# Kernel optimization log

Hardware: AMD Instinct MI355X
Metric: run time of the kernel (lower is better)

The kernel has to match this reference:

```python
import jax, jax.numpy as jnp
import numpy as np

N_NODES = 65536
N_EDGES = 1048576
IN_FEATS = 128
H1 = 128
H2 = 256
N_CLASSES = 16


def setup_inputs() -> dict:
    key = jax.random.key(0)
    ks = jax.random.split(key, 12)
    s = 0.05
    x = jax.random.normal(ks[0], (N_NODES, IN_FEATS), dtype=jnp.float32)
    src = jax.random.randint(ks[1], (N_EDGES,), 0, N_NODES, dtype=jnp.int32)
    dst = jax.random.randint(ks[2], (N_EDGES,), 0, N_NODES, dtype=jnp.int32)
    # SAGEConv('pool') params: fc_pool (bias), fc_self (no bias), fc_neigh (no bias), output bias
    Wp = jax.random.normal(ks[3], (H1, IN_FEATS), dtype=jnp.float32) * s
    bp = jnp.zeros((H1,), dtype=jnp.float32)
    Ws = jax.random.normal(ks[4], (H1, IN_FEATS), dtype=jnp.float32) * s
    Wn = jax.random.normal(ks[5], (H1, H1), dtype=jnp.float32) * s
    bn = jnp.zeros((H1,), dtype=jnp.float32)
    # MLP head
    W1 = jax.random.normal(ks[6], (H2, H1), dtype=jnp.float32) * s
    b1 = jnp.zeros((H2,), dtype=jnp.float32)
    W2 = jax.random.normal(ks[7], (N_CLASSES, H2), dtype=jnp.float32) * s
    b2 = jnp.zeros((N_CLASSES,), dtype=jnp.float32)
    return {"x": x, "Wp": Wp, "bp": bp, "Ws": Ws, "Wn": Wn, "bn": bn,
            "W1": W1, "b1": b1, "W2": W2, "b2": b2, "src": src, "dst": dst}


def reference(x, Wp, bp, Ws, Wn, bn, W1, b1, W2, b2, src, dst):
    N = x.shape[0]
    # SAGEConv 'pool': per-edge MLP on gathered source features, segment-max over dst
    m = jax.nn.relu(x[src] @ Wp.T + bp)              # [E, H1]
    pooled = jax.ops.segment_max(m, dst, num_segments=N)  # [N, H1], -inf for isolated
    pooled = jnp.where(jnp.isneginf(pooled), 0.0, pooled)
    h = x @ Ws.T + pooled @ Wn.T + bn                # combine self + neigh
    h = jax.nn.leaky_relu(h)                         # slope 0.01 matches torch default
    h = jax.nn.leaky_relu(h @ W1.T + b1)
    # dropout is identity in eval mode
    h = jax.nn.sigmoid(h @ W2.T + b2)
    return h
```

## Files before the change

kernel.cpp:

```cpp
#include <hip/hip_runtime.h>
#include <cstdint>
#include <cstddef>

typedef __attribute__((ext_vector_type(8))) __bf16 bf16x8;
typedef __attribute__((ext_vector_type(4))) float f32x4;

union bf8pack { unsigned short u[8]; bf16x8 v; uint4 q; };

#define BCAP 768

static __device__ __forceinline__ unsigned short f2b(float f) {
    union { float f; unsigned int u; } v; v.f = f;
    unsigned int u = v.u;
    unsigned int r = (u + 0x7fffu + ((u >> 16) & 1u)) >> 16;
    return (unsigned short)r;
}

static __device__ __forceinline__ bf16x8 cvt8(const float* __restrict__ p) {
    float4 f0 = *(const float4*)p;
    float4 f1 = *(const float4*)(p + 4);
    bf8pack pk;
    pk.u[0] = f2b(f0.x); pk.u[1] = f2b(f0.y);
    pk.u[2] = f2b(f0.z); pk.u[3] = f2b(f0.w);
    pk.u[4] = f2b(f1.x); pk.u[5] = f2b(f1.y);
    pk.u[6] = f2b(f1.z); pk.u[7] = f2b(f1.w);
    return pk.v;
}

static __device__ __forceinline__ unsigned int pkmax(unsigned int a, unsigned int b) {
    unsigned int d;
    asm("v_pk_max_u16 %0, %1, %2" : "=v"(d) : "v"(a), "v"(b));
    return d;
}

__global__ __launch_bounds__(256) void mega0(
    const int* __restrict__ src, const int* __restrict__ dst,
    int* __restrict__ bcnt, unsigned int* __restrict__ pairs,
    const float* __restrict__ x, const float* __restrict__ Wp,
    const float* __restrict__ bp,
    const float* __restrict__ Ws, const float* __restrict__ Wn,
    const float* __restrict__ W1, const float* __restrict__ W2,
    unsigned short* __restrict__ Wcat, unsigned short* __restrict__ W1_b,
    unsigned short* __restrict__ W2_b, unsigned short* __restrict__ y,
    unsigned short* __restrict__ xb)
{
    const int tid = threadIdx.x;
    const int bx = (int)blockIdx.x;

    if (bx < 512) {
        const int bm = bx;
        const int w  = tid >> 6;
        const int wm = w & 1, wn = w >> 1;
        const int l  = tid & 63;
        const int lr = l & 15, quad = l >> 4;
        const int m0 = bm * 128 + wm * 64;
        const int n0 = wn * 64;

        f32x4 acc[4][4];
#pragma unroll
        for (int i = 0; i < 4; i++)
#pragma unroll
            for (int j = 0; j < 4; j++) acc[i][j] = (f32x4){0.f, 0.f, 0.f, 0.f};

        const float* Apf = x  + (size_t)(m0 + lr) * 128 + quad * 8;
        const float* Bpf = Wp + (size_t)(n0 + lr) * 128 + quad * 8;

#pragma unroll
        for (int ks = 0; ks < 4; ks++) {
            bf16x8 af[4], bf[4];
#pragma unroll
            for (int i = 0; i < 4; i++) {
                const float* p = Apf + (size_t)i * 16 * 128 + ks * 32;
                float4 f0 = *(const float4*)p;
                float4 f1 = *(const float4*)(p + 4);
                bf8pack pk;
                pk.u[0] = f2b(f0.x); pk.u[1] = f2b(f0.y);
                pk.u[2] = f2b(f0.z); pk.u[3] = f2b(f0.w);
                pk.u[4] = f2b(f1.x); pk.u[5] = f2b(f1.y);
                pk.u[6] = f2b(f1.z); pk.u[7] = f2b(f1.w);
                af[i] = pk.v;
                if (wn == 0)
                    *(uint4*)(xb + (size_t)(m0 + lr + i * 16) * 128 + ks * 32 + quad * 8) = pk.q;
            }
#pragma unroll
            for (int i = 0; i < 4; i++)
                bf[i] = cvt8(Bpf + (size_t)i * 16 * 128 + ks * 32);
#pragma unroll
            for (int mi = 0; mi < 4; mi++)
#pragma unroll
                for (int ni = 0; ni < 4; ni++)
                    acc[mi][ni] = __builtin_amdgcn_mfma_f32_16x16x32_bf16(
                        af[mi], bf[ni], acc[mi][ni], 0, 0, 0);
        }

#pragma unroll
        for (int ni = 0; ni < 4; ni++) {
            const int col = n0 + ni * 16 + lr;
            const float bv = bp[col];
#pragma unroll
            for (int mi = 0; mi < 4; mi++) {
#pragma unroll
                for (int r = 0; r < 4; r++) {
                    const int row = m0 + mi * 16 + quad * 4 + r;
                    float v = acc[mi][ni][r] + bv;
                    v = v > 0.f ? v : 0.f;
                    y[(size_t)row * 128 + col] = f2b(v);
                }
            }
        }
        return;
    }

    if (bx < 784) {
        int i = (bx - 512) * 256 + tid;
        if (i < 32768) {
            int o = i >> 8, k = i & 255;
            Wcat[i] = f2b(k < 128 ? Ws[o * 128 + k] : Wn[o * 128 + (k - 128)]);
        } else if (i < 65536) {
            W1_b[i - 32768] = f2b(W1[i - 32768]);
        } else {
            W2_b[i - 65536] = f2b(W2[i - 65536]);
        }
        return;
    }

    __shared__ int h[2048];
    __shared__ int base_l[2048];
    __shared__ int cnt[2048];
    for (int i = tid; i < 2048; i += 256) { h[i] = 0; cnt[i] = 0; }
    __syncthreads();
    const int base = (bx - 784) * 4096;
    int d_r[16], s_r[16];
    const int4* s4 = (const int4*)(src + base);
    const int4* d4 = (const int4*)(dst + base);
#pragma unroll
    for (int i = 0; i < 4; i++) {
        int4 dv = d4[tid + i * 256];
        int4 sv = s4[tid + i * 256];
        d_r[i * 4 + 0] = dv.x; d_r[i * 4 + 1] = dv.y;
        d_r[i * 4 + 2] = dv.z; d_r[i * 4 + 3] = dv.w;
        s_r[i * 4 + 0] = sv.x; s_r[i * 4 + 1] = sv.y;
        s_r[i * 4 + 2] = sv.z; s_r[i * 4 + 3] = sv.w;
    }
#pragma unroll
    for (int i = 0; i < 16; i++)
        atomicAdd(&h[((unsigned)d_r[i]) >> 5], 1);
    __syncthreads();
    for (int i = tid; i < 2048; i += 256)
        base_l[i] = h[i] ? (i * BCAP + atomicAdd(&bcnt[i], h[i])) : 0;
    __syncthreads();
#pragma unroll
    for (int i = 0; i < 16; i++) {
        int b = ((unsigned)d_r[i]) >> 5;
        int pos = base_l[b] + atomicAdd(&cnt[b], 1);
        if (pos < (b + 1) * BCAP)
            pairs[pos] = ((unsigned)s_r[i] << 5) | ((unsigned)d_r[i] & 31u);
    }
}

__global__ __launch_bounds__(256, 4) void megaB(
    const unsigned int* __restrict__ yu, const int* __restrict__ bcnt,
    const unsigned int* __restrict__ pairs,
    const unsigned short* __restrict__ xb,
    const unsigned short* __restrict__ Wcat, const float* __restrict__ bn,
    const unsigned short* __restrict__ W1_b, const float* __restrict__ b1,
    const unsigned short* __restrict__ W2_b, const float* __restrict__ b2,
    float* __restrict__ out)
{
    __shared__ unsigned short S[32 * 264];
    __shared__ unsigned int xbS[32 * 64];
    __shared__ unsigned short ldsSrc[1024];
    __shared__ int bin[32], offl[32], cnt2[32];
    unsigned int* PS = (unsigned int*)&S[32 * 136];

    const int b = blockIdx.x;
    const int tid = threadIdx.x;
    const int w = tid >> 6, l = tid & 63;
    const int lr = l & 15, quad = l >> 4;
    const int row0 = b * 32;

    {
        const int tr = tid >> 3;
        const int tc = (tid & 7) * 8;
        const unsigned int* g = (const unsigned int*)(xb + (size_t)(row0 + tr) * 128) + tc;
        uint4 va = *(const uint4*)g;
        uint4 vb = *(const uint4*)(g + 4);
        const int mask = (tr & 7) << 2;
        *(uint4*)&xbS[tr * 64 + (tc ^ mask)]       = va;
        *(uint4*)&xbS[tr * 64 + ((tc + 4) ^ mask)] = vb;
    }

    if (tid < 32) { bin[tid] = 0; cnt2[tid] = 0; }
    __syncthreads();
    const int beg = b * BCAP;
    int nb = bcnt[b]; nb = nb < BCAP ? nb : BCAP;

    for (int i = tid; i < nb; i += 256)
        atomicAdd(&bin[pairs[beg + i] & 31u], 1);
    __syncthreads();

    if (tid < 32) {
        int c = bin[tid];
        int p = (c + 7) & ~7;
        int s = p;
#pragma unroll
        for (int d = 1; d < 32; d <<= 1) {
            int t = __shfl_up(s, d);
            if (tid >= d) s += t;
        }
        offl[tid] = s - p;
    }
    __syncthreads();

    for (int i = tid; i < nb; i += 256) {
        unsigned int p = pairs[beg + i];
        int d = p & 31u;
        int slot = offl[d] + atomicAdd(&cnt2[d], 1);
        ldsSrc[slot] = (unsigned short)(p >> 5);
    }
    __syncthreads();

    if (tid < 32) {
        int c = bin[tid];
        if (c > 0) {
            int o = offl[tid];
            unsigned short last = ldsSrc[o + c - 1];
            int p = (c + 7) & ~7;
            for (int k = c; k < p; k++) ldsSrc[o + k] = last;
        }
    }
    __syncthreads();

    const unsigned int* __restrict__ ylane = yu + l;
#pragma unroll
    for (int g = 0; g < 2; g++) {
        const int n0 = w * 8 + g * 4;
        unsigned int acc[4] = {0u, 0u, 0u, 0u};
        int e0a[4], rka[4];
#pragma unroll
        for (int k = 0; k < 4; k++) {
            e0a[k] = offl[n0 + k];
            rka[k] = (bin[n0 + k] + 7) >> 3;
        }
        int maxr = rka[0];
#pragma unroll
        for (int k = 1; k < 4; k++) maxr = rka[k] > maxr ? rka[k] : maxr;

        for (int r = 0; r < maxr; r++) {
            unsigned int vv[4][8];
#pragma unroll
            for (int k = 0; k < 4; k++) {
                if (r < rka[k]) {
                    uint4 sv = *(const uint4*)&ldsSrc[e0a[k] + r * 8];
                    vv[k][0] = ylane[(size_t)(sv.x & 0xffffu) << 6];
                    vv[k][1] = ylane[(size_t)(sv.x >> 16) << 6];
                    vv[k][2] = ylane[(size_t)(sv.y & 0xffffu) << 6];
                    vv[k][3] = ylane[(size_t)(sv.y >> 16) << 6];
                    vv[k][4] = ylane[(size_t)(sv.z & 0xffffu) << 6];
                    vv[k][5] = ylane[(size_t)(sv.z >> 16) << 6];
                    vv[k][6] = ylane[(size_t)(sv.w & 0xffffu) << 6];
                    vv[k][7] = ylane[(size_t)(sv.w >> 16) << 6];
                }
            }
#pragma unroll
            for (int k = 0; k < 4; k++) {
                if (r < rka[k]) {
                    unsigned int m01 = pkmax(vv[k][0], vv[k][1]);
                    unsigned int m23 = pkmax(vv[k][2], vv[k][3]);
                    unsigned int m45 = pkmax(vv[k][4], vv[k][5]);
                    unsigned int m67 = pkmax(vv[k][6], vv[k][7]);
                    acc[k] = pkmax(acc[k], pkmax(pkmax(m01, m23), pkmax(m45, m67)));
                }
            }
        }
#pragma unroll
        for (int k = 0; k < 4; k++) {
            const int n = n0 + k;
            PS[n * 64 + (l ^ ((n & 7) << 2))] = acc[k];
        }
    }
    __syncthreads();

    {
        f32x4 acc[2][2];
#pragma unroll
        for (int i = 0; i < 2; i++)
#pragma unroll
            for (int j = 0; j < 2; j++) acc[i][j] = (f32x4){0.f, 0.f, 0.f, 0.f};

        const unsigned short* Bp = Wcat + (size_t)(w * 32 + lr) * 256 + quad * 8;

#pragma unroll
        for (int ks = 0; ks < 8; ks++) {
            bf16x8 af[2], bf[2];
            if (ks < 4) {
#pragma unroll
                for (int i = 0; i < 2; i++) {
                    const int row = i * 16 + lr;
                    const int c0 = ks * 16 + quad * 4;
                    af[i] = *(const bf16x8*)&xbS[row * 64 + (c0 ^ ((row & 7) << 2))];
                }
            } else {
#pragma unroll
                for (int i = 0; i < 2; i++) {
                    const int row = i * 16 + lr;
                    const int c0 = (ks - 4) * 16 + quad * 4;
                    af[i] = *(const bf16x8*)&PS[row * 64 + (c0 ^ ((row & 7) << 2))];
                }
            }
#pragma unroll
            for (int i = 0; i < 2; i++)
                bf[i] = *(const bf16x8*)(Bp + (size_t)i * 16 * 256 + ks * 32);
#pragma unroll
            for (int mi = 0; mi < 2; mi++)
#pragma unroll
                for (int ni = 0; ni < 2; ni++)
                    acc[mi][ni] = __builtin_amdgcn_mfma_f32_16x16x32_bf16(
                        af[mi], bf[ni], acc[mi][ni], 0, 0, 0);
        }

#pragma unroll
        for (int ni = 0; ni < 2; ni++) {
            const int col = w * 32 + ni * 16 + lr;
            const float bv = bn[col];
#pragma unroll
            for (int mi = 0; mi < 2; mi++) {
#pragma unroll
                for (int r = 0; r < 4; r++) {
                    const int row = mi * 16 + quad * 4 + r;
                    float v = acc[mi][ni][r] + bv;
                    v = v > 0.f ? v : 0.01f * v;
                    S[row * 136 + col] = f2b(v);
                }
            }
        }
    }
    __syncthreads();

    {
        f32x4 acc[2][4];
#pragma unroll
        for (int i = 0; i < 2; i++)
#pragma unroll
            for (int j = 0; j < 4; j++) acc[i][j] = (f32x4){0.f, 0.f, 0.f, 0.f};

        const unsigned short* Bp = W1_b + (size_t)(w * 64 + lr) * 128 + quad * 8;

#pragma unroll
        for (int ks = 0; ks < 4; ks++) {
            bf16x8 af[2], bfr[4];
#pragma unroll
            for (int i = 0; i < 2; i++)
                af[i] = *(const bf16x8*)&S[(i * 16 + lr) * 136 + ks * 32 + quad * 8];
#pragma unroll
            for (int i = 0; i < 4; i++)
                bfr[i] = *(const bf16x8*)(Bp + (size_t)i * 16 * 128 + ks * 32);
#pragma unroll
            for (int mi = 0; mi < 2; mi++)
#pragma unroll
                for (int ni = 0; ni < 4; ni++)
                    acc[mi][ni] = __builtin_amdgcn_mfma_f32_16x16x32_bf16(
                        af[mi], bfr[ni], acc[mi][ni], 0, 0, 0);
        }
        __syncthreads();

#pragma unroll
        for (int ni = 0; ni < 4; ni++) {
            const int col = w * 64 + ni * 16 + lr;
            const float bv = b1[col];
#pragma unroll
            for (int mi = 0; mi < 2; mi++) {
#pragma unroll
                for (int r = 0; r < 4; r++) {
                    const int row = mi * 16 + quad * 4 + r;
                    float v = acc[mi][ni][r] + bv;
                    v = v > 0.f ? v : 0.01f * v;
                    S[row * 264 + col] = f2b(v);
                }
            }
        }
    }
    __syncthreads();

    if (w < 2) {
        const int m0 = w * 16;
        f32x4 a2 = (f32x4){0.f, 0.f, 0.f, 0.f};
#pragma unroll
        for (int ks = 0; ks < 8; ks++) {
            bf16x8 a = *(const bf16x8*)&S[(m0 + lr) * 264 + ks * 32 + quad * 8];
            bf16x8 bb = *(const bf16x8*)(W2_b + (size_t)lr * 256 + ks * 32 + quad * 8);
            a2 = __builtin_amdgcn_mfma_f32_16x16x32_bf16(a, bb, a2, 0, 0, 0);
        }
        const float bv = b2[lr];
#pragma unroll
        for (int r = 0; r < 4; r++) {
            const int row = row0 + m0 + quad * 4 + r;
            float v = a2[r] + bv;
            out[(size_t)row * 16 + lr] = 1.f / (1.f + __expf(-v));
        }
    }
}

extern "C" void kernel_launch(void* const* d_in, const int* in_sizes, int n_in,
                              void* d_out, int out_size, void* d_ws, size_t ws_size,
                              hipStream_t stream)
{
    const float* x  = (const float*)d_in[0];
    const float* Wp = (const float*)d_in[1];
    const float* bp = (const float*)d_in[2];
    const float* Ws = (const float*)d_in[3];
    const float* Wn = (const float*)d_in[4];
    const float* bn = (const float*)d_in[5];
    const float* W1 = (const float*)d_in[6];
    const float* b1 = (const float*)d_in[7];
    const float* W2 = (const float*)d_in[8];
    const float* b2 = (const float*)d_in[9];
    const int* src  = (const int*)d_in[10];
    const int* dst  = (const int*)d_in[11];
    float* out = (float*)d_out;

    const int N = in_sizes[0] / 128;

    unsigned short* y    = (unsigned short*)d_ws;
    unsigned short* xb   = (unsigned short*)((char*)d_ws + (size_t)16 * 1024 * 1024);
    unsigned short* Wcat = (unsigned short*)((char*)d_ws + (size_t)32 * 1024 * 1024);
    unsigned short* W1_b = Wcat + 32768;
    unsigned short* W2_b = W1_b + 32768;
    int* bcnt = (int*)(W2_b + 4096);
    unsigned int* pairs = (unsigned int*)(bcnt + 2048);

    dim3 blk(256);

    hipMemsetAsync(bcnt, 0, 2048 * sizeof(int), stream);

    mega0<<<1040, blk, 0, stream>>>(src, dst, bcnt, pairs,
                                    x, Wp, bp, Ws, Wn, W1, W2,
                                    Wcat, W1_b, W2_b, y, xb);

    megaB<<<N / 32, blk, 0, stream>>>((const unsigned int*)y, bcnt, pairs,
                                      xb, Wcat, bn, W1_b, b1, W2_b, b2, out);
}
```

Before: 200.0 us.

## Split megaB into 16-node blocks, two blocks per edge bucket

Each megaB block now handles 16 destination nodes instead of 32. Two blocks share one 32-node edge bucket and each filters pairs by a bit of the destination index. This doubles the grid, halves shared memory per block and raises the launch-bounds occupancy target, so there is more parallelism for the latency-bound gather-max. In exchange, both blocks scan the full bucket of pairs, the weight loads from global memory for the GEMMs are repeated per 16 rows, and the tail MLP runs on a single wave.

```diff
diff --git a/kernel.cpp b/kernel.cpp
--- a/kernel.cpp
+++ b/kernel.cpp
@@ -158,7 +158,7 @@
     }
 }
 
-__global__ __launch_bounds__(256, 4) void megaB(
+__global__ __launch_bounds__(256, 5) void megaB(
     const unsigned int* __restrict__ yu, const int* __restrict__ bcnt,
     const unsigned int* __restrict__ pairs,
     const unsigned short* __restrict__ xb,
@@ -167,44 +167,46 @@
     const unsigned short* __restrict__ W2_b, const float* __restrict__ b2,
     float* __restrict__ out)
 {
-    __shared__ unsigned short S[32 * 264];
-    __shared__ unsigned int xbS[32 * 64];
-    __shared__ unsigned short ldsSrc[1024];
-    __shared__ int bin[32], offl[32], cnt2[32];
-    unsigned int* PS = (unsigned int*)&S[32 * 136];
+    __shared__ unsigned short S[16 * 264];
+    __shared__ unsigned int xbS[16 * 64];
+    __shared__ unsigned short ldsSrc[768];
+    __shared__ int bin[16], offl[16], cnt2[16];
+    unsigned int* PS = (unsigned int*)&S[16 * 136];
 
     const int b = blockIdx.x;
     const int tid = threadIdx.x;
     const int w = tid >> 6, l = tid & 63;
     const int lr = l & 15, quad = l >> 4;
-    const int row0 = b * 32;
+    const int row0 = b * 16;
 
     {
-        const int tr = tid >> 3;
-        const int tc = (tid & 7) * 8;
+        const int tr = tid >> 4;
+        const int tc = (tid & 15) * 4;
         const unsigned int* g = (const unsigned int*)(xb + (size_t)(row0 + tr) * 128) + tc;
         uint4 va = *(const uint4*)g;
-        uint4 vb = *(const uint4*)(g + 4);
         const int mask = (tr & 7) << 2;
-        *(uint4*)&xbS[tr * 64 + (tc ^ mask)]       = va;
-        *(uint4*)&xbS[tr * 64 + ((tc + 4) ^ mask)] = vb;
-    }
-
-    if (tid < 32) { bin[tid] = 0; cnt2[tid] = 0; }
-    __syncthreads();
-    const int beg = b * BCAP;
-    int nb = bcnt[b]; nb = nb < BCAP ? nb : BCAP;
-
-    for (int i = tid; i < nb; i += 256)
-        atomicAdd(&bin[pairs[beg + i] & 31u], 1);
-    __syncthreads();
-
-    if (tid < 32) {
+        *(uint4*)&xbS[tr * 64 + (tc ^ mask)] = va;
+    }
+
+    if (tid < 16) { bin[tid] = 0; cnt2[tid] = 0; }
+    __syncthreads();
+    const int bucket = b >> 1, half = b & 1;
+    const int beg = bucket * BCAP;
+    int nb = bcnt[bucket]; nb = nb < BCAP ? nb : BCAP;
+
+    for (int i = tid; i < nb; i += 256) {
+        unsigned int p = pairs[beg + i];
+        if ((int)((p >> 4) & 1u) == half)
+            atomicAdd(&bin[p & 15u], 1);
+    }
+    __syncthreads();
+
+    if (tid < 16) {
         int c = bin[tid];
         int p = (c + 7) & ~7;
         int s = p;
 #pragma unroll
-        for (int d = 1; d < 32; d <<= 1) {
+        for (int d = 1; d < 16; d <<= 1) {
             int t = __shfl_up(s, d);
             if (tid >= d) s += t;
         }
@@ -214,27 +216,29 @@
 
     for (int i = tid; i < nb; i += 256) {
         unsigned int p = pairs[beg + i];
-        int d = p & 31u;
-        int slot = offl[d] + atomicAdd(&cnt2[d], 1);
-        ldsSrc[slot] = (unsigned short)(p >> 5);
-    }
-    __syncthreads();
-
-    if (tid < 32) {
+        if ((int)((p >> 4) & 1u) == half) {
+            int d = p & 15u;
+            int slot = offl[d] + atomicAdd(&cnt2[d], 1);
+            if (slot < 768) ldsSrc[slot] = (unsigned short)(p >> 5);
+        }
+    }
+    __syncthreads();
+
+    if (tid < 16) {
         int c = bin[tid];
         if (c > 0) {
             int o = offl[tid];
             unsigned short last = ldsSrc[o + c - 1];
             int p = (c + 7) & ~7;
-            for (int k = c; k < p; k++) ldsSrc[o + k] = last;
+            for (int k = c; k < p; k++)
+                if (o + k < 768) ldsSrc[o + k] = last;
         }
     }
     __syncthreads();
 
     const unsigned int* __restrict__ ylane = yu + l;
-#pragma unroll
-    for (int g = 0; g < 2; g++) {
-        const int n0 = w * 8 + g * 4;
+    {
+        const int n0 = w * 4;
         unsigned int acc[4] = {0u, 0u, 0u, 0u};
         int e0a[4], rka[4];
 #pragma unroll
@@ -282,41 +286,29 @@
     __syncthreads();
 
     {
-        f32x4 acc[2][2];
-#pragma unroll
-        for (int i = 0; i < 2; i++)
-#pragma unroll
-            for (int j = 0; j < 2; j++) acc[i][j] = (f32x4){0.f, 0.f, 0.f, 0.f};
+        f32x4 acc[2];
+#pragma unroll
+        for (int i = 0; i < 2; i++) acc[i] = (f32x4){0.f, 0.f, 0.f, 0.f};
 
         const unsigned short* Bp = Wcat + (size_t)(w * 32 + lr) * 256 + quad * 8;
 
 #pragma unroll
         for (int ks = 0; ks < 8; ks++) {
-            bf16x8 af[2], bf[2];
+            bf16x8 af, bf[2];
             if (ks < 4) {
-#pragma unroll
-                for (int i = 0; i < 2; i++) {
-                    const int row = i * 16 + lr;
-                    const int c0 = ks * 16 + quad * 4;
-                    af[i] = *(const bf16x8*)&xbS[row * 64 + (c0 ^ ((row & 7) << 2))];
-                }
+                const int c0 = ks * 16 + quad * 4;
+                af = *(const bf16x8*)&xbS[lr * 64 + (c0 ^ ((lr & 7) << 2))];
             } else {
-#pragma unroll
-                for (int i = 0; i < 2; i++) {
-                    const int row = i * 16 + lr;
-                    const int c0 = (ks - 4) * 16 + quad * 4;
-                    af[i] = *(const bf16x8*)&PS[row * 64 + (c0 ^ ((row & 7) << 2))];
-                }
+                const int c0 = (ks - 4) * 16 + quad * 4;
+                af = *(const bf16x8*)&PS[lr * 64 + (c0 ^ ((lr & 7) << 2))];
             }
 #pragma unroll
             for (int i = 0; i < 2; i++)
                 bf[i] = *(const bf16x8*)(Bp + (size_t)i * 16 * 256 + ks * 32);
 #pragma unroll
-            for (int mi = 0; mi < 2; mi++)
-#pragma unroll
-                for (int ni = 0; ni < 2; ni++)
-                    acc[mi][ni] = __builtin_amdgcn_mfma_f32_16x16x32_bf16(
-                        af[mi], bf[ni], acc[mi][ni], 0, 0, 0);
+            for (int ni = 0; ni < 2; ni++)
+                acc[ni] = __builtin_amdgcn_mfma_f32_16x16x32_bf16(
+                    af, bf[ni], acc[ni], 0, 0, 0);
         }
 
 #pragma unroll
@@ -324,43 +316,34 @@
             const int col = w * 32 + ni * 16 + lr;
             const float bv = bn[col];
 #pragma unroll
-            for (int mi = 0; mi < 2; mi++) {
-#pragma unroll
-                for (int r = 0; r < 4; r++) {
-                    const int row = mi * 16 + quad * 4 + r;
-                    float v = acc[mi][ni][r] + bv;
-                    v = v > 0.f ? v : 0.01f * v;
-                    S[row * 136 + col] = f2b(v);
-                }
+            for (int r = 0; r < 4; r++) {
+                const int row = quad * 4 + r;
+                float v = acc[ni][r] + bv;
+                v = v > 0.f ? v : 0.01f * v;
+                S[row * 136 + col] = f2b(v);
             }
         }
     }
     __syncthreads();
 
     {
-        f32x4 acc[2][4];
-#pragma unroll
-        for (int i = 0; i < 2; i++)
-#pragma unroll
-            for (int j = 0; j < 4; j++) acc[i][j] = (f32x4){0.f, 0.f, 0.f, 0.f};
+        f32x4 acc[4];
+#pragma unroll
+        for (int j = 0; j < 4; j++) acc[j] = (f32x4){0.f, 0.f, 0.f, 0.f};
 
         const unsigned short* Bp = W1_b + (size_t)(w * 64 + lr) * 128 + quad * 8;
 
 #pragma unroll
         for (int ks = 0; ks < 4; ks++) {
-            bf16x8 af[2], bfr[4];
-#pragma unroll
-            for (int i = 0; i < 2; i++)
-                af[i] = *(const bf16x8*)&S[(i * 16 + lr) * 136 + ks * 32 + quad * 8];
+            bf16x8 af, bfr[4];
+            af = *(const bf16x8*)&S[lr * 136 + ks * 32 + quad * 8];
 #pragma unroll
             for (int i = 0; i < 4; i++)
                 bfr[i] = *(const bf16x8*)(Bp + (size_t)i * 16 * 128 + ks * 32);
 #pragma unroll
-            for (int mi = 0; mi < 2; mi++)
-#pragma unroll
-                for (int ni = 0; ni < 4; ni++)
-                    acc[mi][ni] = __builtin_amdgcn_mfma_f32_16x16x32_bf16(
-                        af[mi], bfr[ni], acc[mi][ni], 0, 0, 0);
+            for (int ni = 0; ni < 4; ni++)
+                acc[ni] = __builtin_amdgcn_mfma_f32_16x16x32_bf16(
+                    af, bfr[ni], acc[ni], 0, 0, 0);
         }
         __syncthreads();
 
@@ -369,32 +352,28 @@
             const int col = w * 64 + ni * 16 + lr;
             const float bv = b1[col];
 #pragma unroll
-            for (int mi = 0; mi < 2; mi++) {
-#pragma unroll
-                for (int r = 0; r < 4; r++) {
-                    const int row = mi * 16 + quad * 4 + r;
-                    float v = acc[mi][ni][r] + bv;
-                    v = v > 0.f ? v : 0.01f * v;
-                    S[row * 264 + col] = f2b(v);
-                }
-            }
-        }
-    }
-    __syncthreads();
-
-    if (w < 2) {
-        const int m0 = w * 16;
+            for (int r = 0; r < 4; r++) {
+                const int row = quad * 4 + r;
+                float v = acc[ni][r] + bv;
+                v = v > 0.f ? v : 0.01f * v;
+                S[row * 264 + col] = f2b(v);
+            }
+        }
+    }
+    __syncthreads();
+
+    if (w == 0) {
         f32x4 a2 = (f32x4){0.f, 0.f, 0.f, 0.f};
 #pragma unroll
         for (int ks = 0; ks < 8; ks++) {
-            bf16x8 a = *(const bf16x8*)&S[(m0 + lr) * 264 + ks * 32 + quad * 8];
+            bf16x8 a = *(const bf16x8*)&S[lr * 264 + ks * 32 + quad * 8];
             bf16x8 bb = *(const bf16x8*)(W2_b + (size_t)lr * 256 + ks * 32 + quad * 8);
             a2 = __builtin_amdgcn_mfma_f32_16x16x32_bf16(a, bb, a2, 0, 0, 0);
         }
         const float bv = b2[lr];
 #pragma unroll
         for (int r = 0; r < 4; r++) {
-            const int row = row0 + m0 + quad * 4 + r;
+            const int row = row0 + quad * 4 + r;
             float v = a2[r] + bv;
             out[(size_t)row * 16 + lr] = 1.f / (1.f + __expf(-v));
         }
@@ -437,6 +416,6 @@
                                     x, Wp, bp, Ws, Wn, W1, W2,
                                     Wcat, W1_b, W2_b, y, xb);
 
-    megaB<<<N / 32, blk, 0, stream>>>((const unsigned int*)y, bcnt, pairs,
+    megaB<<<N / 16, blk, 0, stream>>>((const unsigned int*)y, bcnt, pairs,
                                       xb, Wcat, bn, W1_b, b1, W2_b, b2, out);
 }
```

New measurement: 222.9 us. 1.11x slower.
